# Performance work log

Hardware: AMD Instinct MI355X
Metric: run time of the kernel (lower is better)

The kernel has to match this reference:

```python
import jax, jax.numpy as jnp
import numpy as np

N = 50000
E = 800000
IN = 128
H = 128
C = 64
BN_EPS = 1e-5


def gcn_conv(x, W, b, src, dst, n_nodes):
    # GCNConv: add self-loops, symmetric normalization D^-1/2 (A+I) D^-1/2, linear, bias
    deg = jax.ops.segment_sum(jnp.ones_like(dst, dtype=x.dtype), dst, num_segments=n_nodes)
    dinv = jnp.where(deg > 0, jax.lax.rsqrt(deg), jnp.zeros_like(deg))
    norm = dinv[src] * dinv[dst]                      # [E+N]
    h = x @ W                                         # [N, out]
    agg = jax.ops.segment_sum(norm[:, None] * h[src], dst, num_segments=n_nodes)
    return agg + b


def batch_norm_eval(x, gamma, beta, mean, var):
    return gamma * (x - mean) * jax.lax.rsqrt(var + BN_EPS) + beta


def setup_inputs() -> dict:
    key = jax.random.key(0)
    ks = jax.random.split(key, 16)
    inp = {
        "x": jax.random.normal(ks[0], (N, IN), dtype=jnp.float32),
        "edge_index": jax.random.randint(ks[1], (2, E), 0, N, dtype=jnp.int64),
        "W1": jax.random.normal(ks[2], (IN, H), dtype=jnp.float32) / np.sqrt(IN),
        "b1": jnp.zeros((H,), dtype=jnp.float32),
        "g1": jnp.ones((H,), dtype=jnp.float32),
        "be1": jnp.zeros((H,), dtype=jnp.float32),
        "m1": jax.random.normal(ks[3], (H,), dtype=jnp.float32) * 0.1,
        "v1": jax.random.uniform(ks[4], (H,), dtype=jnp.float32, minval=0.5, maxval=1.5),
        "W2": jax.random.normal(ks[5], (H, H), dtype=jnp.float32) / np.sqrt(H),
        "b2": jnp.zeros((H,), dtype=jnp.float32),
        "g2": jnp.ones((H,), dtype=jnp.float32),
        "be2": jnp.zeros((H,), dtype=jnp.float32),
        "m2": jax.random.normal(ks[6], (H,), dtype=jnp.float32) * 0.1,
        "v2": jax.random.uniform(ks[7], (H,), dtype=jnp.float32, minval=0.5, maxval=1.5),
        "W3": jax.random.normal(ks[8], (H, C), dtype=jnp.float32) / np.sqrt(H),
        "b3": jnp.zeros((C,), dtype=jnp.float32),
    }
    return inp


def reference(x, edge_index, W1, b1, g1, be1, m1, v1, W2, b2, g2, be2, m2, v2, W3, b3):
    # add self loops once (shared across layers, GCNConv cached=True)
    loop = jnp.arange(N, dtype=edge_index.dtype)
    src = jnp.concatenate([edge_index[0], loop])
    dst = jnp.concatenate([edge_index[1], loop])

    h = gcn_conv(x, W1, b1, src, dst, N)
    h = jax.nn.relu(batch_norm_eval(h, g1, be1, m1, v1))  # eval mode: dropout is identity
    h = gcn_conv(h, W2, b2, src, dst, N)
    h = jax.nn.relu(batch_norm_eval(h, g2, be2, m2, v2))
    out = gcn_conv(h, W3, b3, src, dst, N)
    return out
```

## Files before the change

kernel.cpp:

```cpp
#include <hip/hip_runtime.h>


#define NCHUNK 256
#define BSHIFT 8
#define BWID 256
#define NSLAB 8
#define SSHIFT 13
#define ECAP 8192

typedef __attribute__((ext_vector_type(8))) short bf16x8;
typedef __attribute__((ext_vector_type(4))) float f32x4;

__device__ __forceinline__ float blo(unsigned p) { return __uint_as_float(p << 16); }
__device__ __forceinline__ float bhi(unsigned p) { return __uint_as_float(p & 0xffff0000u); }
__device__ __forceinline__ unsigned short f2b(float f) {
  unsigned u = __float_as_uint(f);
  unsigned r = (u + 0x7fffu + ((u >> 16) & 1u)) >> 16;
  return (unsigned short)r;
}

__global__ void wprep_kernel(const float* __restrict__ W1, const float* __restrict__ W2,
                             const float* __restrict__ W3,
                             const float* __restrict__ b1, const float* __restrict__ g1,
                             const float* __restrict__ be1, const float* __restrict__ m1,
                             const float* __restrict__ v1,
                             const float* __restrict__ b2, const float* __restrict__ g2,
                             const float* __restrict__ be2, const float* __restrict__ m2,
                             const float* __restrict__ v2,
                             unsigned short* __restrict__ Wt1,
                             unsigned short* __restrict__ Wt2,
                             unsigned short* __restrict__ Wt3,
                             float* __restrict__ sc1, float* __restrict__ sh1,
                             float* __restrict__ sc2, float* __restrict__ sh2) {
  int i = blockIdx.x * 256 + threadIdx.x;
  if (i < 16384) {
    int k = i >> 7, c = i & 127;
    Wt1[c * 128 + k] = f2b(W1[i]);
  } else if (i < 32768) {
    int j = i - 16384; int k = j >> 7, c = j & 127;
    Wt2[c * 128 + k] = f2b(W2[j]);
  } else if (i < 40960) {
    int j = i - 32768; int k = j >> 6, c = j & 63;
    Wt3[c * 128 + k] = f2b(W3[j]);
  } else if (i < 41088) {
    int c = i - 40960;
    float s = g1[c] * rsqrtf(v1[c] + 1e-5f);
    sc1[c] = s; sh1[c] = (b1[c] - m1[c]) * s + be1[c];
  } else if (i < 41216) {
    int c = i - 41088;
    float s = g2[c] * rsqrtf(v2[c] + 1e-5f);
    sc2[c] = s; sh2[c] = (b2[c] - m2[c]) * s + be2[c];
  }
}

__global__ __launch_bounds__(256) void bin_hist_kernel(
    const int* __restrict__ ei32, const long long* __restrict__ ei64,
    int* __restrict__ counts, int E, int nkeys) {
  __shared__ int hist[2048];
  __shared__ int s_is32;
  int k = blockIdx.x, t = threadIdx.x;
  for (int i = t; i < nkeys; i += 256) hist[i] = 0;
  if (t == 0) s_is32 = 0;
  int CH = (E + NCHUNK - 1) / NCHUNK;
  int e0 = k * CH, e1 = min(e0 + CH, E);
  __syncthreads();
  if (t < 64 && e0 + t < E && ei32[2 * (e0 + t) + 1] != 0) atomicOr(&s_is32, 1);
  __syncthreads();
  int is32 = s_is32;
  for (int e = e0 + t; e < e1; e += 256) {
    int s, d;
    if (is32) { s = ei32[e]; d = ei32[E + e]; }
    else      { s = (int)ei64[e]; d = (int)ei64[E + e]; }
    atomicAdd(&hist[((d >> BSHIFT) << 3) | (s >> SSHIFT)], 1);
  }
  __syncthreads();
  for (int i = t; i < nkeys; i += 256) counts[i * NCHUNK + k] = hist[i];
}

template <int CHUNK>
__global__ __launch_bounds__(256) void scan_partial_kernel(
    const int* __restrict__ src, int* __restrict__ bsum, int n) {
  __shared__ int wsum[4];
  constexpr int EL = CHUNK / 256;
  int b = blockIdx.x, t = threadIdx.x;
  int lane = t & 63, wv = t >> 6;
  int s = 0;
  int i0 = b * CHUNK + t * EL;
#pragma unroll
  for (int q = 0; q < EL / 4; ++q) {
    int i = i0 + q * 4;
    if (i + 3 < n) {
      int4 d4 = *(const int4*)&src[i];
      s += d4.x + d4.y + d4.z + d4.w;
    } else {
      for (int r = 0; r < 4; ++r) if (i + r < n) s += src[i + r];
    }
  }
#pragma unroll
  for (int off = 32; off; off >>= 1) s += __shfl_xor(s, off);
  if (lane == 0) wsum[wv] = s;
  __syncthreads();
  if (t == 0) bsum[b] = wsum[0] + wsum[1] + wsum[2] + wsum[3];
}

template <int CHUNK>
__global__ __launch_bounds__(256) void scan_write_kernel(
    const int* __restrict__ src, const int* __restrict__ bsum,
    int* __restrict__ outp, int n, int nb) {
  constexpr int EL = CHUNK / 256;
  __shared__ int woff[4];
  __shared__ int s_boff;
  int b = blockIdx.x, t = threadIdx.x;
  int lane = t & 63, wv = t >> 6;
  if (t < 64) {
    int v = (t < nb) ? bsum[t] : 0;
    int ic = v;
#pragma unroll
    for (int off = 1; off < 64; off <<= 1) {
      int u = __shfl_up(ic, off);
      if (t >= off) ic += u;
    }
    if (t == b) s_boff = ic - v;
    if (b == nb - 1 && t == 63) outp[n] = ic;
  }
  int vals[EL];
  int i0 = b * CHUNK + t * EL;
#pragma unroll
  for (int q = 0; q < EL / 4; ++q) {
    int i = i0 + q * 4;
    int4 d4 = make_int4(0, 0, 0, 0);
    if (i + 3 < n) d4 = *(const int4*)&src[i];
    else {
      if (i < n) d4.x = src[i];
      if (i + 1 < n) d4.y = src[i + 1];
      if (i + 2 < n) d4.z = src[i + 2];
    }
    vals[q * 4] = d4.x; vals[q * 4 + 1] = d4.y;
    vals[q * 4 + 2] = d4.z; vals[q * 4 + 3] = d4.w;
  }
  int tsum = 0;
#pragma unroll
  for (int q = 0; q < EL; ++q) tsum += vals[q];
  int inc = tsum;
#pragma unroll
  for (int off = 1; off < 64; off <<= 1) {
    int u = __shfl_up(inc, off);
    if (lane >= off) inc += u;
  }
  if (lane == 63) woff[wv] = inc;
  __syncthreads();
  if (t == 0) {
    int r = 0;
#pragma unroll
    for (int w = 0; w < 4; ++w) { int sw = woff[w]; woff[w] = r; r += sw; }
  }
  __syncthreads();
  int p = inc - tsum + woff[wv] + s_boff;
#pragma unroll
  for (int q = 0; q < EL; ++q) {
    int i = i0 + q;
    if (i < n) outp[i] = p;
    p += vals[q];
  }
}

__global__ __launch_bounds__(256) void bin_scatter_kernel(
    const int* __restrict__ ei32, const long long* __restrict__ ei64,
    const int* __restrict__ offs, unsigned* __restrict__ pairs, int E, int nkeys) {
  __shared__ int cur[2048];
  __shared__ int s_is32;
  int k = blockIdx.x, t = threadIdx.x;
  for (int i = t; i < nkeys; i += 256) cur[i] = offs[i * NCHUNK + k];
  if (t == 0) s_is32 = 0;
  int CH = (E + NCHUNK - 1) / NCHUNK;
  int e0 = k * CH, e1 = min(e0 + CH, E);
  __syncthreads();
  if (t < 64 && e0 + t < E && ei32[2 * (e0 + t) + 1] != 0) atomicOr(&s_is32, 1);
  __syncthreads();
  int is32 = s_is32;
  for (int e = e0 + t; e < e1; e += 256) {
    int s, d;
    if (is32) { s = ei32[e]; d = ei32[E + e]; }
    else      { s = (int)ei64[e]; d = (int)ei64[E + e]; }
    int pos = atomicAdd(&cur[((d >> BSHIFT) << 3) | (s >> SSHIFT)], 1);
    pairs[pos] = (unsigned)s | ((unsigned)(d & (BWID - 1)) << 20);
  }
}

__global__ __launch_bounds__(256) void bucket_p1_kernel(
    const unsigned* __restrict__ pairs, const int* __restrict__ offs,
    int* __restrict__ rowptr, float* __restrict__ dinv, int E, int n) {
  __shared__ int deg[BWID];
  __shared__ int woff[4];
  int b = blockIdx.x, t = threadIdx.x;
  int lane = t & 63, wv = t >> 6;
  deg[t] = 0;
  __syncthreads();
  int basep = offs[b * NSLAB * NCHUNK];
  int endp = offs[(b + 1) * NSLAB * NCHUNK];
  for (int i = basep + t; i < endp; i += 256)
    atomicAdd(&deg[pairs[i] >> 20], 1);
  __syncthreads();
  int dg = deg[t];
  int inc = dg + 1;
#pragma unroll
  for (int off = 1; off < 64; off <<= 1) {
    int u = __shfl_up(inc, off);
    if (lane >= off) inc += u;
  }
  if (lane == 63) woff[wv] = inc;
  __syncthreads();
  if (t == 0) {
    int r = 0;
#pragma unroll
    for (int w = 0; w < 4; ++w) { int sw = woff[w]; woff[w] = r; r += sw; }
  }
  __syncthreads();
  int exc = inc - (dg + 1) + woff[wv];
  int cwbase = basep + b * BWID;
  int idx = b * BWID + t;
  if (idx < n) {
    rowptr[idx] = cwbase + exc;
    dinv[idx] = rsqrtf((float)(dg + 1));
  }
  if (b == 0 && t == 0) rowptr[n] = E + n;
}

__global__ __launch_bounds__(256) void bucket_p2_kernel(
    const unsigned* __restrict__ pairs, const int* __restrict__ offs,
    const int* __restrict__ rowptr, const float* __restrict__ dinv,
    uint2* __restrict__ cw, int E, int n) {
  __shared__ int cur[BWID];
  __shared__ float dsl[BWID];
  __shared__ int stage_s[ECAP];
  __shared__ float stage_w[ECAP];
  int b = blockIdx.x, t = threadIdx.x;
  int basep = offs[b * NSLAB * NCHUNK];
  int endp = offs[(b + 1) * NSLAB * NCHUNK];
  int cwbase = basep + b * BWID;
  int idx = b * BWID + t;
  int nreal = min(n - b * BWID, BWID);
  float dv = (t < nreal) ? dinv[idx] : 0.f;
  dsl[t] = dv;
  cur[t] = (t < nreal) ? rowptr[idx] - cwbase : 0;
  __syncthreads();
  if (t < nreal) {
    int pos = atomicAdd(&cur[t], 1);
    if (pos < ECAP) { stage_s[pos] = idx; stage_w[pos] = dv * dv; }
    else cw[cwbase + pos] = make_uint2((unsigned)idx, __float_as_uint(dv * dv));
  }
  __syncthreads();
  for (int i = basep + t; i < endp; i += 256) {
    unsigned p = pairs[i];
    int s = (int)(p & 0xFFFFFu);
    int dl = (int)(p >> 20);
    int pos = atomicAdd(&cur[dl], 1);
    float w = dinv[s] * dsl[dl];
    if (pos < ECAP) { stage_s[pos] = s; stage_w[pos] = w; }
    else cw[cwbase + pos] = make_uint2((unsigned)s, __float_as_uint(w));
  }
  __syncthreads();
  int nE = (endp - basep) + nreal;
  int lim = min(nE, ECAP);
  for (int i = t; i < lim; i += 256)
    cw[cwbase + i] = make_uint2((unsigned)stage_s[i], __float_as_uint(stage_w[i]));
}

template <int HOUT, int ABF16>
__global__ __launch_bounds__(256) void mgemm_kernel(
    const void* __restrict__ Ain, const unsigned short* __restrict__ Wt,
    unsigned short* __restrict__ Y, int n) {
  constexpr int NT = HOUT;
  __shared__ unsigned char AsB[64 * 256];
  __shared__ unsigned char BsB[NT * 256];
  int t = threadIdx.x;
  int row0 = blockIdx.x * 64;

  if constexpr (ABF16) {
    const unsigned short* A = (const unsigned short*)Ain;
#pragma unroll
    for (int jj = 0; jj < 4; ++jj) {
      int f = t + 256 * jj; int r = f >> 4, kq = f & 15;
      uint4 v = make_uint4(0, 0, 0, 0);
      if (row0 + r < n) v = *(const uint4*)&A[(size_t)(row0 + r) * 128 + kq * 8];
      *(uint4*)&AsB[r * 256 + ((kq * 16) ^ ((r & 15) << 4))] = v;
    }
  } else {
    const float* A = (const float*)Ain;
#pragma unroll
    for (int jj = 0; jj < 8; ++jj) {
      int f = t + 256 * jj; int r = f >> 5, kq = f & 31;
      float4 v = make_float4(0.f, 0.f, 0.f, 0.f);
      if (row0 + r < n) v = *(const float4*)&A[(size_t)(row0 + r) * 128 + kq * 4];
      unsigned two0 = (unsigned)f2b(v.x) | ((unsigned)f2b(v.y) << 16);
      unsigned two1 = (unsigned)f2b(v.z) | ((unsigned)f2b(v.w) << 16);
      uint2 o = make_uint2(two0, two1);
      *(uint2*)&AsB[r * 256 + ((kq * 8) ^ ((r & 15) << 4))] = o;
    }
  }
#pragma unroll
  for (int jj = 0; jj < NT / 16; ++jj) {
    int f = t + 256 * jj; int c = f >> 4, kq = f & 15;
    uint4 v = *(const uint4*)&Wt[(size_t)c * 128 + kq * 8];
    *(uint4*)&BsB[c * 256 + ((kq * 16) ^ ((c & 15) << 4))] = v;
  }
  __syncthreads();

  int l = t & 63, wid = t >> 6;
  constexpr int WC = NT / 2;
  constexpr int NI = WC / 16;
  int wr = (wid >> 1) * 32, wc = (wid & 1) * WC;
  int lr = l & 15, lk = (l >> 4) * 16;

  f32x4 acc[2][NI] = {};
#pragma unroll
  for (int ks = 0; ks < 4; ++ks) {
    bf16x8 a[2], b[NI];
#pragma unroll
    for (int mi = 0; mi < 2; ++mi) {
      int r = wr + mi * 16 + lr;
      a[mi] = *(const bf16x8*)&AsB[r * 256 + ((ks * 64 + lk) ^ ((r & 15) << 4))];
    }
#pragma unroll
    for (int ni = 0; ni < NI; ++ni) {
      int c = wc + ni * 16 + lr;
      b[ni] = *(const bf16x8*)&BsB[c * 256 + ((ks * 64 + lk) ^ ((c & 15) << 4))];
    }
#pragma unroll
    for (int mi = 0; mi < 2; ++mi)
#pragma unroll
      for (int ni = 0; ni < NI; ++ni)
        acc[mi][ni] = __builtin_amdgcn_mfma_f32_16x16x32_bf16(a[mi], b[ni],
                                                              acc[mi][ni], 0, 0, 0);
  }

#pragma unroll
  for (int mi = 0; mi < 2; ++mi) {
#pragma unroll
    for (int reg = 0; reg < 4; ++reg) {
      int gr = row0 + wr + mi * 16 + (l >> 4) * 4 + reg;
      if (gr < n) {
#pragma unroll
        for (int ni = 0; ni < NI; ++ni) {
          int gc = wc + ni * 16 + lr;
          Y[(size_t)gr * HOUT + gc] = f2b(acc[mi][ni][reg]);
        }
      }
    }
  }
}

template <int HOUT, bool BN, bool OUTBF>
__global__ __launch_bounds__(256) void agg_kernel(
    const unsigned short* __restrict__ h, const int* __restrict__ rowptr,
    const uint2* __restrict__ cw,
    const float* __restrict__ sc, const float* __restrict__ sh,
    void* __restrict__ out, int n_nodes) {
  int n = (blockIdx.x * blockDim.x + threadIdx.x) >> 6;
  if (n >= n_nodes) return;
  int lane = threadIdx.x & 63;
  constexpr int GL = HOUT / 8;
  constexpr int NPH = 64 / GL;
  int phase = lane / GL;
  int sub = lane & (GL - 1);
  const uint4* hu = (const uint4*)h;

  int beg = rowptr[n], end = rowptr[n + 1];
  float a[8] = {0.f, 0.f, 0.f, 0.f, 0.f, 0.f, 0.f, 0.f};

  int j = beg + phase;
  for (; j + 3 * NPH < end; j += 4 * NPH) {
    uint2 e0 = cw[j], e1 = cw[j + NPH], e2 = cw[j + 2 * NPH], e3 = cw[j + 3 * NPH];
    uint4 h0 = hu[(size_t)e0.x * GL + sub];
    uint4 h1 = hu[(size_t)e1.x * GL + sub];
    uint4 h2 = hu[(size_t)e2.x * GL + sub];
    uint4 h3 = hu[(size_t)e3.x * GL + sub];
    float w0 = __uint_as_float(e0.y), w1 = __uint_as_float(e1.y);
    float w2 = __uint_as_float(e2.y), w3 = __uint_as_float(e3.y);
    a[0] = fmaf(w0, blo(h0.x), a[0]); a[1] = fmaf(w0, bhi(h0.x), a[1]);
    a[2] = fmaf(w0, blo(h0.y), a[2]); a[3] = fmaf(w0, bhi(h0.y), a[3]);
    a[4] = fmaf(w0, blo(h0.z), a[4]); a[5] = fmaf(w0, bhi(h0.z), a[5]);
    a[6] = fmaf(w0, blo(h0.w), a[6]); a[7] = fmaf(w0, bhi(h0.w), a[7]);
    a[0] = fmaf(w1, blo(h1.x), a[0]); a[1] = fmaf(w1, bhi(h1.x), a[1]);
    a[2] = fmaf(w1, blo(h1.y), a[2]); a[3] = fmaf(w1, bhi(h1.y), a[3]);
    a[4] = fmaf(w1, blo(h1.z), a[4]); a[5] = fmaf(w1, bhi(h1.z), a[5]);
    a[6] = fmaf(w1, blo(h1.w), a[6]); a[7] = fmaf(w1, bhi(h1.w), a[7]);
    a[0] = fmaf(w2, blo(h2.x), a[0]); a[1] = fmaf(w2, bhi(h2.x), a[1]);
    a[2] = fmaf(w2, blo(h2.y), a[2]); a[3] = fmaf(w2, bhi(h2.y), a[3]);
    a[4] = fmaf(w2, blo(h2.z), a[4]); a[5] = fmaf(w2, bhi(h2.z), a[5]);
    a[6] = fmaf(w2, blo(h2.w), a[6]); a[7] = fmaf(w2, bhi(h2.w), a[7]);
    a[0] = fmaf(w3, blo(h3.x), a[0]); a[1] = fmaf(w3, bhi(h3.x), a[1]);
    a[2] = fmaf(w3, blo(h3.y), a[2]); a[3] = fmaf(w3, bhi(h3.y), a[3]);
    a[4] = fmaf(w3, blo(h3.z), a[4]); a[5] = fmaf(w3, bhi(h3.z), a[5]);
    a[6] = fmaf(w3, blo(h3.w), a[6]); a[7] = fmaf(w3, bhi(h3.w), a[7]);
  }
  for (; j < end; j += NPH) {
    uint2 e = cw[j];
    uint4 hv = hu[(size_t)e.x * GL + sub];
    float w = __uint_as_float(e.y);
    a[0] = fmaf(w, blo(hv.x), a[0]); a[1] = fmaf(w, bhi(hv.x), a[1]);
    a[2] = fmaf(w, blo(hv.y), a[2]); a[3] = fmaf(w, bhi(hv.y), a[3]);
    a[4] = fmaf(w, blo(hv.z), a[4]); a[5] = fmaf(w, bhi(hv.z), a[5]);
    a[6] = fmaf(w, blo(hv.w), a[6]); a[7] = fmaf(w, bhi(hv.w), a[7]);
  }

#pragma unroll
  for (int q = 0; q < 8; ++q) {
    a[q] += __shfl_xor(a[q], 32);
    a[q] += __shfl_xor(a[q], 16);
    if constexpr (NPH == 8) a[q] += __shfl_xor(a[q], 8);
  }
  if (phase != 0) return;

  int c0 = sub * 8;
  float y[8];
#pragma unroll
  for (int q = 0; q < 8; ++q) {
    if constexpr (BN) y[q] = fmaxf(fmaf(a[q], sc[c0 + q], sh[c0 + q]), 0.f);
    else y[q] = a[q] + sh[c0 + q];
  }
  if constexpr (OUTBF) {
    uint4 o;
    o.x = (unsigned)f2b(y[0]) | ((unsigned)f2b(y[1]) << 16);
    o.y = (unsigned)f2b(y[2]) | ((unsigned)f2b(y[3]) << 16);
    o.z = (unsigned)f2b(y[4]) | ((unsigned)f2b(y[5]) << 16);
    o.w = (unsigned)f2b(y[6]) | ((unsigned)f2b(y[7]) << 16);
    ((uint4*)out)[(size_t)n * GL + sub] = o;
  } else {
    float* op = (float*)out + (size_t)n * HOUT + c0;
    float4 o0; o0.x = y[0]; o0.y = y[1]; o0.z = y[2]; o0.w = y[3];
    float4 o1; o1.x = y[4]; o1.y = y[5]; o1.z = y[6]; o1.w = y[7];
    *(float4*)op = o0;
    *(float4*)(op + 4) = o1;
  }
}

extern "C" void kernel_launch(void* const* d_in, const int* in_sizes, int n_in,
                              void* d_out, int out_size, void* d_ws, size_t ws_size,
                              hipStream_t stream) {
  const float* x = (const float*)d_in[0];
  const int* ei32 = (const int*)d_in[1];
  const long long* ei64 = (const long long*)d_in[1];
  const float* W1 = (const float*)d_in[2];
  const float* b1 = (const float*)d_in[3];
  const float* g1 = (const float*)d_in[4];
  const float* be1 = (const float*)d_in[5];
  const float* m1 = (const float*)d_in[6];
  const float* v1 = (const float*)d_in[7];
  const float* W2 = (const float*)d_in[8];
  const float* b2 = (const float*)d_in[9];
  const float* g2 = (const float*)d_in[10];
  const float* be2 = (const float*)d_in[11];
  const float* m2 = (const float*)d_in[12];
  const float* v2 = (const float*)d_in[13];
  const float* W3 = (const float*)d_in[14];
  const float* b3 = (const float*)d_in[15];

  const int N = in_sizes[0] / 128;
  const int E = in_sizes[1] / 2;
  const int NBK = (N + BWID - 1) / BWID;
  const int NKEYS = NBK * NSLAB;
  const int NC = NKEYS * NCHUNK;

  char* ws = (char*)d_ws;
  size_t off = 0;
  auto alloc = [&](size_t bytes) -> void* {
    void* p = ws + off;
    off = (off + bytes + 255) & ~(size_t)255;
    return p;
  };
  float* dinv = (float*)alloc((size_t)N * 4);
  int* rowptr = (int*)alloc((size_t)(N + 1) * 4);
  int* counts = (int*)alloc((size_t)NC * 4);
  int* offs = (int*)alloc((size_t)(NC + 1) * 4);
  unsigned* pairs = (unsigned*)alloc((size_t)E * 4);
  uint2* cw = (uint2*)alloc((size_t)(E + N) * 8);
  int* bsum = (int*)alloc(64 * 4);
  unsigned short* wt1 = (unsigned short*)alloc(128 * 128 * 2);
  unsigned short* wt2 = (unsigned short*)alloc(128 * 128 * 2);
  unsigned short* wt3 = (unsigned short*)alloc(128 * 64 * 2);
  float* sc1 = (float*)alloc(128 * 4);
  float* sh1 = (float*)alloc(128 * 4);
  float* sc2 = (float*)alloc(128 * 4);
  float* sh2 = (float*)alloc(128 * 4);
  unsigned short* hbuf = (unsigned short*)alloc((size_t)N * 128 * 2);
  unsigned short* ybuf = (unsigned short*)alloc((size_t)N * 128 * 2);
  (void)ws_size;

  wprep_kernel<<<161, 256, 0, stream>>>(W1, W2, W3, b1, g1, be1, m1, v1,
                                        b2, g2, be2, m2, v2,
                                        wt1, wt2, wt3, sc1, sh1, sc2, sh2);

  bin_hist_kernel<<<NCHUNK, 256, 0, stream>>>(ei32, ei64, counts, E, NKEYS);
  int nbC = (NC + 8191) / 8192;
  scan_partial_kernel<8192><<<nbC, 256, 0, stream>>>(counts, bsum, NC);
  scan_write_kernel<8192><<<nbC, 256, 0, stream>>>(counts, bsum, offs, NC, nbC);
  bin_scatter_kernel<<<NCHUNK, 256, 0, stream>>>(ei32, ei64, offs, pairs, E, NKEYS);
  bucket_p1_kernel<<<NBK, 256, 0, stream>>>(pairs, offs, rowptr, dinv, E, N);
  bucket_p2_kernel<<<NBK, 256, 0, stream>>>(pairs, offs, rowptr, dinv, cw, E, N);

  int gb = (N + 63) / 64;
  int ab = (N + 3) / 4;

  mgemm_kernel<128, 0><<<gb, 256, 0, stream>>>(x, wt1, hbuf, N);
  agg_kernel<128, true, true><<<ab, 256, 0, stream>>>(hbuf, rowptr, cw,
                                                      sc1, sh1, ybuf, N);
  mgemm_kernel<128, 1><<<gb, 256, 0, stream>>>(ybuf, wt2, hbuf, N);
  agg_kernel<128, true, true><<<ab, 256, 0, stream>>>(hbuf, rowptr, cw,
                                                      sc2, sh2, ybuf, N);
  mgemm_kernel<64, 1><<<gb, 256, 0, stream>>>(ybuf, wt3, hbuf, N);
  agg_kernel<64, false, false><<<ab, 256, 0, stream>>>(hbuf, rowptr, cw,
                                                       nullptr, b3, d_out, N);
}
```

Baseline: 184.0 us.

## Restructure SpMM aggregation to broadcast edge lists via readlane, lanes span features

The aggregation kernel stops splitting edges across lane groups that each load 16-byte vectors. Instead the wavefront loads up to 64 edge entries cooperatively and broadcasts each one with readlane, so every lane gathers 4 bytes of the neighbour row and keeps only two accumulators. This removes the cross-lane shuffle reduction and the register pressure of eight accumulators per lane. The cost is narrower per-lane loads, more gather instructions per edge, and serial processing of neighbours within a wavefront. The histogram shift is also renamed to a macro without changing its value.

```diff
diff --git a/kernel.cpp b/kernel.cpp
--- a/kernel.cpp
+++ b/kernel.cpp
@@ -6,6 +6,7 @@
 #define BWID 256
 #define NSLAB 8
 #define SSHIFT 13
+#define SLOG 3
 #define ECAP 8192
 
 typedef __attribute__((ext_vector_type(8))) short bf16x8;
@@ -71,7 +72,7 @@
     int s, d;
     if (is32) { s = ei32[e]; d = ei32[E + e]; }
     else      { s = (int)ei64[e]; d = (int)ei64[E + e]; }
-    atomicAdd(&hist[((d >> BSHIFT) << 3) | (s >> SSHIFT)], 1);
+    atomicAdd(&hist[((d >> BSHIFT) << SLOG) | (s >> SSHIFT)], 1);
   }
   __syncthreads();
   for (int i = t; i < nkeys; i += 256) counts[i * NCHUNK + k] = hist[i];
@@ -182,7 +183,7 @@
     int s, d;
     if (is32) { s = ei32[e]; d = ei32[E + e]; }
     else      { s = (int)ei64[e]; d = (int)ei64[E + e]; }
-    int pos = atomicAdd(&cur[((d >> BSHIFT) << 3) | (s >> SSHIFT)], 1);
+    int pos = atomicAdd(&cur[((d >> BSHIFT) << SLOG) | (s >> SSHIFT)], 1);
     pairs[pos] = (unsigned)s | ((unsigned)(d & (BWID - 1)) << 20);
   }
 }
@@ -359,79 +360,103 @@
   int n = (blockIdx.x * blockDim.x + threadIdx.x) >> 6;
   if (n >= n_nodes) return;
   int lane = threadIdx.x & 63;
-  constexpr int GL = HOUT / 8;
-  constexpr int NPH = 64 / GL;
-  int phase = lane / GL;
-  int sub = lane & (GL - 1);
-  const uint4* hu = (const uint4*)h;
-
+  const unsigned* hu = (const unsigned*)h;
   int beg = rowptr[n], end = rowptr[n + 1];
-  float a[8] = {0.f, 0.f, 0.f, 0.f, 0.f, 0.f, 0.f, 0.f};
-
-  int j = beg + phase;
-  for (; j + 3 * NPH < end; j += 4 * NPH) {
-    uint2 e0 = cw[j], e1 = cw[j + NPH], e2 = cw[j + 2 * NPH], e3 = cw[j + 3 * NPH];
-    uint4 h0 = hu[(size_t)e0.x * GL + sub];
-    uint4 h1 = hu[(size_t)e1.x * GL + sub];
-    uint4 h2 = hu[(size_t)e2.x * GL + sub];
-    uint4 h3 = hu[(size_t)e3.x * GL + sub];
-    float w0 = __uint_as_float(e0.y), w1 = __uint_as_float(e1.y);
-    float w2 = __uint_as_float(e2.y), w3 = __uint_as_float(e3.y);
-    a[0] = fmaf(w0, blo(h0.x), a[0]); a[1] = fmaf(w0, bhi(h0.x), a[1]);
-    a[2] = fmaf(w0, blo(h0.y), a[2]); a[3] = fmaf(w0, bhi(h0.y), a[3]);
-    a[4] = fmaf(w0, blo(h0.z), a[4]); a[5] = fmaf(w0, bhi(h0.z), a[5]);
-    a[6] = fmaf(w0, blo(h0.w), a[6]); a[7] = fmaf(w0, bhi(h0.w), a[7]);
-    a[0] = fmaf(w1, blo(h1.x), a[0]); a[1] = fmaf(w1, bhi(h1.x), a[1]);
-    a[2] = fmaf(w1, blo(h1.y), a[2]); a[3] = fmaf(w1, bhi(h1.y), a[3]);
-    a[4] = fmaf(w1, blo(h1.z), a[4]); a[5] = fmaf(w1, bhi(h1.z), a[5]);
-    a[6] = fmaf(w1, blo(h1.w), a[6]); a[7] = fmaf(w1, bhi(h1.w), a[7]);
-    a[0] = fmaf(w2, blo(h2.x), a[0]); a[1] = fmaf(w2, bhi(h2.x), a[1]);
-    a[2] = fmaf(w2, blo(h2.y), a[2]); a[3] = fmaf(w2, bhi(h2.y), a[3]);
-    a[4] = fmaf(w2, blo(h2.z), a[4]); a[5] = fmaf(w2, bhi(h2.z), a[5]);
-    a[6] = fmaf(w2, blo(h2.w), a[6]); a[7] = fmaf(w2, bhi(h2.w), a[7]);
-    a[0] = fmaf(w3, blo(h3.x), a[0]); a[1] = fmaf(w3, bhi(h3.x), a[1]);
-    a[2] = fmaf(w3, blo(h3.y), a[2]); a[3] = fmaf(w3, bhi(h3.y), a[3]);
-    a[4] = fmaf(w3, blo(h3.z), a[4]); a[5] = fmaf(w3, bhi(h3.z), a[5]);
-    a[6] = fmaf(w3, blo(h3.w), a[6]); a[7] = fmaf(w3, bhi(h3.w), a[7]);
-  }
-  for (; j < end; j += NPH) {
-    uint2 e = cw[j];
-    uint4 hv = hu[(size_t)e.x * GL + sub];
-    float w = __uint_as_float(e.y);
-    a[0] = fmaf(w, blo(hv.x), a[0]); a[1] = fmaf(w, bhi(hv.x), a[1]);
-    a[2] = fmaf(w, blo(hv.y), a[2]); a[3] = fmaf(w, bhi(hv.y), a[3]);
-    a[4] = fmaf(w, blo(hv.z), a[4]); a[5] = fmaf(w, bhi(hv.z), a[5]);
-    a[6] = fmaf(w, blo(hv.w), a[6]); a[7] = fmaf(w, bhi(hv.w), a[7]);
-  }
-
-#pragma unroll
-  for (int q = 0; q < 8; ++q) {
-    a[q] += __shfl_xor(a[q], 32);
-    a[q] += __shfl_xor(a[q], 16);
-    if constexpr (NPH == 8) a[q] += __shfl_xor(a[q], 8);
-  }
-  if (phase != 0) return;
-
-  int c0 = sub * 8;
-  float y[8];
-#pragma unroll
-  for (int q = 0; q < 8; ++q) {
-    if constexpr (BN) y[q] = fmaxf(fmaf(a[q], sc[c0 + q], sh[c0 + q]), 0.f);
-    else y[q] = a[q] + sh[c0 + q];
-  }
-  if constexpr (OUTBF) {
-    uint4 o;
-    o.x = (unsigned)f2b(y[0]) | ((unsigned)f2b(y[1]) << 16);
-    o.y = (unsigned)f2b(y[2]) | ((unsigned)f2b(y[3]) << 16);
-    o.z = (unsigned)f2b(y[4]) | ((unsigned)f2b(y[5]) << 16);
-    o.w = (unsigned)f2b(y[6]) | ((unsigned)f2b(y[7]) << 16);
-    ((uint4*)out)[(size_t)n * GL + sub] = o;
+  int deg = end - beg;
+
+  float acc0 = 0.f, acc1 = 0.f;
+
+  if constexpr (HOUT == 128) {
+    for (int j0 = 0; j0 < deg; j0 += 64) {
+      int ii = beg + j0 + lane;
+      ii = ii < end ? ii : end - 1;
+      uint2 sv = cw[ii];
+      int cnt = min(64, deg - j0);
+      int j = 0;
+      for (; j + 3 < cnt; j += 4) {
+        unsigned s0 = __builtin_amdgcn_readlane(sv.x, j);
+        unsigned u0 = __builtin_amdgcn_readlane(sv.y, j);
+        unsigned s1 = __builtin_amdgcn_readlane(sv.x, j + 1);
+        unsigned u1 = __builtin_amdgcn_readlane(sv.y, j + 1);
+        unsigned s2 = __builtin_amdgcn_readlane(sv.x, j + 2);
+        unsigned u2 = __builtin_amdgcn_readlane(sv.y, j + 2);
+        unsigned s3 = __builtin_amdgcn_readlane(sv.x, j + 3);
+        unsigned u3 = __builtin_amdgcn_readlane(sv.y, j + 3);
+        unsigned v0 = hu[(size_t)s0 * 64 + lane];
+        unsigned v1 = hu[(size_t)s1 * 64 + lane];
+        unsigned v2 = hu[(size_t)s2 * 64 + lane];
+        unsigned v3 = hu[(size_t)s3 * 64 + lane];
+        float w0 = __uint_as_float(u0), w1 = __uint_as_float(u1);
+        float w2 = __uint_as_float(u2), w3 = __uint_as_float(u3);
+        acc0 = fmaf(w0, blo(v0), acc0); acc1 = fmaf(w0, bhi(v0), acc1);
+        acc0 = fmaf(w1, blo(v1), acc0); acc1 = fmaf(w1, bhi(v1), acc1);
+        acc0 = fmaf(w2, blo(v2), acc0); acc1 = fmaf(w2, bhi(v2), acc1);
+        acc0 = fmaf(w3, blo(v3), acc0); acc1 = fmaf(w3, bhi(v3), acc1);
+      }
+      for (; j < cnt; ++j) {
+        unsigned s = __builtin_amdgcn_readlane(sv.x, j);
+        unsigned u = __builtin_amdgcn_readlane(sv.y, j);
+        unsigned v = hu[(size_t)s * 64 + lane];
+        float w = __uint_as_float(u);
+        acc0 = fmaf(w, blo(v), acc0);
+        acc1 = fmaf(w, bhi(v), acc1);
+      }
+    }
+    int c0 = lane * 2;
+    float y0, y1;
+    if constexpr (BN) {
+      y0 = fmaxf(fmaf(acc0, sc[c0], sh[c0]), 0.f);
+      y1 = fmaxf(fmaf(acc1, sc[c0 + 1], sh[c0 + 1]), 0.f);
+    } else {
+      y0 = acc0 + sh[c0];
+      y1 = acc1 + sh[c0 + 1];
+    }
+    if constexpr (OUTBF) {
+      unsigned pk = (unsigned)f2b(y0) | ((unsigned)f2b(y1) << 16);
+      ((unsigned*)out)[(size_t)n * 64 + lane] = pk;
+    } else {
+      float2 o; o.x = y0; o.y = y1;
+      *(float2*)&((float*)out)[(size_t)n * 128 + c0] = o;
+    }
   } else {
-    float* op = (float*)out + (size_t)n * HOUT + c0;
-    float4 o0; o0.x = y[0]; o0.y = y[1]; o0.z = y[2]; o0.w = y[3];
-    float4 o1; o1.x = y[4]; o1.y = y[5]; o1.z = y[6]; o1.w = y[7];
-    *(float4*)op = o0;
-    *(float4*)(op + 4) = o1;
+    int half = lane >> 5, hl = lane & 31;
+    for (int j0 = 0; j0 < deg; j0 += 64) {
+      int ii = beg + j0 + lane;
+      ii = ii < end ? ii : end - 1;
+      uint2 sv = cw[ii];
+      int cnt = min(64, deg - j0);
+      for (int j = 0; j < cnt; j += 2) {
+        unsigned sA = __builtin_amdgcn_readlane(sv.x, j);
+        unsigned uA = __builtin_amdgcn_readlane(sv.y, j);
+        int j1 = (j + 1 < cnt) ? j + 1 : j;
+        unsigned sB = __builtin_amdgcn_readlane(sv.x, j1);
+        unsigned uB = (j + 1 < cnt) ? __builtin_amdgcn_readlane(sv.y, j1) : 0u;
+        unsigned s = half ? sB : sA;
+        float w = __uint_as_float(half ? uB : uA);
+        unsigned v = hu[(size_t)s * 32 + hl];
+        acc0 = fmaf(w, blo(v), acc0);
+        acc1 = fmaf(w, bhi(v), acc1);
+      }
+    }
+    acc0 += __shfl_xor(acc0, 32);
+    acc1 += __shfl_xor(acc1, 32);
+    if (half != 0) return;
+    int c0 = hl * 2;
+    float y0, y1;
+    if constexpr (BN) {
+      y0 = fmaxf(fmaf(acc0, sc[c0], sh[c0]), 0.f);
+      y1 = fmaxf(fmaf(acc1, sc[c0 + 1], sh[c0 + 1]), 0.f);
+    } else {
+      y0 = acc0 + sh[c0];
+      y1 = acc1 + sh[c0 + 1];
+    }
+    if constexpr (OUTBF) {
+      unsigned pk = (unsigned)f2b(y0) | ((unsigned)f2b(y1) << 16);
+      ((unsigned*)out)[(size_t)n * 32 + hl] = pk;
+    } else {
+      float2 o; o.x = y0; o.y = y1;
+      *(float2*)&((float*)out)[(size_t)n * 64 + c0] = o;
+    }
   }
 }
 
```

Result: slower. 195.1 us (+6.0%).

## Split aggregation by column groups and drop source-slab binning of edges

Applied to the files above, without the earlier changes.

The aggregation kernel now divides the feature columns into 8 column groups, with 8 consecutive blocks handling the same nodes in different column groups. Each lane gathers one 32-bit word (two bf16 values) per edge instead of a 16-byte vector. The likely intent is to localise the gathered slice of h per column group in cache and to spread work more evenly across blocks. Edge binning is simplified to bin by destination bucket only, removing the source-slab sub-keys, which shrinks the histogram and scan sizes. The trade-off is that each edge list is re-read once per column group, the gathers become narrow, and source locality within a destination bucket is lost.

```diff
diff --git a/kernel.cpp b/kernel.cpp
--- a/kernel.cpp
+++ b/kernel.cpp
@@ -4,8 +4,6 @@
 #define NCHUNK 256
 #define BSHIFT 8
 #define BWID 256
-#define NSLAB 8
-#define SSHIFT 13
 #define ECAP 8192
 
 typedef __attribute__((ext_vector_type(8))) short bf16x8;
@@ -55,11 +53,11 @@
 
 __global__ __launch_bounds__(256) void bin_hist_kernel(
     const int* __restrict__ ei32, const long long* __restrict__ ei64,
-    int* __restrict__ counts, int E, int nkeys) {
-  __shared__ int hist[2048];
+    int* __restrict__ counts, int E, int nbk) {
+  __shared__ int hist[BWID];
   __shared__ int s_is32;
   int k = blockIdx.x, t = threadIdx.x;
-  for (int i = t; i < nkeys; i += 256) hist[i] = 0;
+  hist[t] = 0;
   if (t == 0) s_is32 = 0;
   int CH = (E + NCHUNK - 1) / NCHUNK;
   int e0 = k * CH, e1 = min(e0 + CH, E);
@@ -68,13 +66,11 @@
   __syncthreads();
   int is32 = s_is32;
   for (int e = e0 + t; e < e1; e += 256) {
-    int s, d;
-    if (is32) { s = ei32[e]; d = ei32[E + e]; }
-    else      { s = (int)ei64[e]; d = (int)ei64[E + e]; }
-    atomicAdd(&hist[((d >> BSHIFT) << 3) | (s >> SSHIFT)], 1);
-  }
-  __syncthreads();
-  for (int i = t; i < nkeys; i += 256) counts[i * NCHUNK + k] = hist[i];
+    int d = is32 ? ei32[E + e] : (int)ei64[E + e];
+    atomicAdd(&hist[d >> BSHIFT], 1);
+  }
+  __syncthreads();
+  if (t < nbk) counts[t * NCHUNK + k] = hist[t];
 }
 
 template <int CHUNK>
@@ -166,11 +162,11 @@
 
 __global__ __launch_bounds__(256) void bin_scatter_kernel(
     const int* __restrict__ ei32, const long long* __restrict__ ei64,
-    const int* __restrict__ offs, unsigned* __restrict__ pairs, int E, int nkeys) {
-  __shared__ int cur[2048];
+    const int* __restrict__ offs, unsigned* __restrict__ pairs, int E, int nbk) {
+  __shared__ int cur[BWID];
   __shared__ int s_is32;
   int k = blockIdx.x, t = threadIdx.x;
-  for (int i = t; i < nkeys; i += 256) cur[i] = offs[i * NCHUNK + k];
+  if (t < nbk) cur[t] = offs[t * NCHUNK + k];
   if (t == 0) s_is32 = 0;
   int CH = (E + NCHUNK - 1) / NCHUNK;
   int e0 = k * CH, e1 = min(e0 + CH, E);
@@ -182,7 +178,7 @@
     int s, d;
     if (is32) { s = ei32[e]; d = ei32[E + e]; }
     else      { s = (int)ei64[e]; d = (int)ei64[E + e]; }
-    int pos = atomicAdd(&cur[((d >> BSHIFT) << 3) | (s >> SSHIFT)], 1);
+    int pos = atomicAdd(&cur[d >> BSHIFT], 1);
     pairs[pos] = (unsigned)s | ((unsigned)(d & (BWID - 1)) << 20);
   }
 }
@@ -196,8 +192,8 @@
   int lane = t & 63, wv = t >> 6;
   deg[t] = 0;
   __syncthreads();
-  int basep = offs[b * NSLAB * NCHUNK];
-  int endp = offs[(b + 1) * NSLAB * NCHUNK];
+  int basep = offs[b * NCHUNK];
+  int endp = offs[(b + 1) * NCHUNK];
   for (int i = basep + t; i < endp; i += 256)
     atomicAdd(&deg[pairs[i] >> 20], 1);
   __syncthreads();
@@ -235,8 +231,8 @@
   __shared__ int stage_s[ECAP];
   __shared__ float stage_w[ECAP];
   int b = blockIdx.x, t = threadIdx.x;
-  int basep = offs[b * NSLAB * NCHUNK];
-  int endp = offs[(b + 1) * NSLAB * NCHUNK];
+  int basep = offs[b * NCHUNK];
+  int endp = offs[(b + 1) * NCHUNK];
   int cwbase = basep + b * BWID;
   int idx = b * BWID + t;
   int nreal = min(n - b * BWID, BWID);
@@ -356,82 +352,70 @@
     const uint2* __restrict__ cw,
     const float* __restrict__ sc, const float* __restrict__ sh,
     void* __restrict__ out, int n_nodes) {
-  int n = (blockIdx.x * blockDim.x + threadIdx.x) >> 6;
-  if (n >= n_nodes) return;
+  constexpr int RWU = HOUT / 2;
+  int grp = blockIdx.x & 7;
+  int blk = blockIdx.x >> 3;
+  int wv = threadIdx.x >> 6;
   int lane = threadIdx.x & 63;
-  constexpr int GL = HOUT / 8;
-  constexpr int NPH = 64 / GL;
-  int phase = lane / GL;
-  int sub = lane & (GL - 1);
-  const uint4* hu = (const uint4*)h;
-
-  int beg = rowptr[n], end = rowptr[n + 1];
-  float a[8] = {0.f, 0.f, 0.f, 0.f, 0.f, 0.f, 0.f, 0.f};
-
-  int j = beg + phase;
-  for (; j + 3 * NPH < end; j += 4 * NPH) {
-    uint2 e0 = cw[j], e1 = cw[j + NPH], e2 = cw[j + 2 * NPH], e3 = cw[j + 3 * NPH];
-    uint4 h0 = hu[(size_t)e0.x * GL + sub];
-    uint4 h1 = hu[(size_t)e1.x * GL + sub];
-    uint4 h2 = hu[(size_t)e2.x * GL + sub];
-    uint4 h3 = hu[(size_t)e3.x * GL + sub];
-    float w0 = __uint_as_float(e0.y), w1 = __uint_as_float(e1.y);
-    float w2 = __uint_as_float(e2.y), w3 = __uint_as_float(e3.y);
-    a[0] = fmaf(w0, blo(h0.x), a[0]); a[1] = fmaf(w0, bhi(h0.x), a[1]);
-    a[2] = fmaf(w0, blo(h0.y), a[2]); a[3] = fmaf(w0, bhi(h0.y), a[3]);
-    a[4] = fmaf(w0, blo(h0.z), a[4]); a[5] = fmaf(w0, bhi(h0.z), a[5]);
-    a[6] = fmaf(w0, blo(h0.w), a[6]); a[7] = fmaf(w0, bhi(h0.w), a[7]);
-    a[0] = fmaf(w1, blo(h1.x), a[0]); a[1] = fmaf(w1, bhi(h1.x), a[1]);
-    a[2] = fmaf(w1, blo(h1.y), a[2]); a[3] = fmaf(w1, bhi(h1.y), a[3]);
-    a[4] = fmaf(w1, blo(h1.z), a[4]); a[5] = fmaf(w1, bhi(h1.z), a[5]);
-    a[6] = fmaf(w1, blo(h1.w), a[6]); a[7] = fmaf(w1, bhi(h1.w), a[7]);
-    a[0] = fmaf(w2, blo(h2.x), a[0]); a[1] = fmaf(w2, bhi(h2.x), a[1]);
-    a[2] = fmaf(w2, blo(h2.y), a[2]); a[3] = fmaf(w2, bhi(h2.y), a[3]);
-    a[4] = fmaf(w2, blo(h2.z), a[4]); a[5] = fmaf(w2, bhi(h2.z), a[5]);
-    a[6] = fmaf(w2, blo(h2.w), a[6]); a[7] = fmaf(w2, bhi(h2.w), a[7]);
-    a[0] = fmaf(w3, blo(h3.x), a[0]); a[1] = fmaf(w3, bhi(h3.x), a[1]);
-    a[2] = fmaf(w3, blo(h3.y), a[2]); a[3] = fmaf(w3, bhi(h3.y), a[3]);
-    a[4] = fmaf(w3, blo(h3.z), a[4]); a[5] = fmaf(w3, bhi(h3.z), a[5]);
-    a[6] = fmaf(w3, blo(h3.w), a[6]); a[7] = fmaf(w3, bhi(h3.w), a[7]);
-  }
-  for (; j < end; j += NPH) {
-    uint2 e = cw[j];
-    uint4 hv = hu[(size_t)e.x * GL + sub];
-    float w = __uint_as_float(e.y);
-    a[0] = fmaf(w, blo(hv.x), a[0]); a[1] = fmaf(w, bhi(hv.x), a[1]);
-    a[2] = fmaf(w, blo(hv.y), a[2]); a[3] = fmaf(w, bhi(hv.y), a[3]);
-    a[4] = fmaf(w, blo(hv.z), a[4]); a[5] = fmaf(w, bhi(hv.z), a[5]);
-    a[6] = fmaf(w, blo(hv.w), a[6]); a[7] = fmaf(w, bhi(hv.w), a[7]);
-  }
-
-#pragma unroll
-  for (int q = 0; q < 8; ++q) {
-    a[q] += __shfl_xor(a[q], 32);
-    a[q] += __shfl_xor(a[q], 16);
-    if constexpr (NPH == 8) a[q] += __shfl_xor(a[q], 8);
-  }
-  if (phase != 0) return;
-
-  int c0 = sub * 8;
-  float y[8];
-#pragma unroll
-  for (int q = 0; q < 8; ++q) {
-    if constexpr (BN) y[q] = fmaxf(fmaf(a[q], sc[c0 + q], sh[c0 + q]), 0.f);
-    else y[q] = a[q] + sh[c0 + q];
-  }
-  if constexpr (OUTBF) {
-    uint4 o;
-    o.x = (unsigned)f2b(y[0]) | ((unsigned)f2b(y[1]) << 16);
-    o.y = (unsigned)f2b(y[2]) | ((unsigned)f2b(y[3]) << 16);
-    o.z = (unsigned)f2b(y[4]) | ((unsigned)f2b(y[5]) << 16);
-    o.w = (unsigned)f2b(y[6]) | ((unsigned)f2b(y[7]) << 16);
-    ((uint4*)out)[(size_t)n * GL + sub] = o;
+  int phase = lane >> 3;
+  int sub = lane & 7;
+  int cg, n0;
+  if constexpr (HOUT == 128) {
+    cg = grp;
+    n0 = blk * 8 + wv * 2;
   } else {
-    float* op = (float*)out + (size_t)n * HOUT + c0;
-    float4 o0; o0.x = y[0]; o0.y = y[1]; o0.z = y[2]; o0.w = y[3];
-    float4 o1; o1.x = y[4]; o1.y = y[5]; o1.z = y[6]; o1.w = y[7];
-    *(float4*)op = o0;
-    *(float4*)(op + 4) = o1;
+    cg = grp >> 1;
+    n0 = (blk * 2 + (grp & 1)) * 8 + wv * 2;
+  }
+  const unsigned* hu = (const unsigned*)h;
+  int cbase = cg * 8;
+
+#pragma unroll
+  for (int ni = 0; ni < 2; ++ni) {
+    int n = n0 + ni;
+    if (n >= n_nodes) continue;
+    int beg = rowptr[n], end = rowptr[n + 1];
+    float a0 = 0.f, a1 = 0.f;
+    for (int j = beg; j < end; j += 32) {
+      int j0 = j + phase, j1 = j0 + 8, j2 = j0 + 16, j3 = j0 + 24;
+      uint2 e0 = cw[j0 < end ? j0 : end - 1];
+      uint2 e1 = cw[j1 < end ? j1 : end - 1];
+      uint2 e2 = cw[j2 < end ? j2 : end - 1];
+      uint2 e3 = cw[j3 < end ? j3 : end - 1];
+      unsigned v0 = hu[(size_t)e0.x * RWU + cbase + sub];
+      unsigned v1 = hu[(size_t)e1.x * RWU + cbase + sub];
+      unsigned v2 = hu[(size_t)e2.x * RWU + cbase + sub];
+      unsigned v3 = hu[(size_t)e3.x * RWU + cbase + sub];
+      float w0 = (j0 < end) ? __uint_as_float(e0.y) : 0.f;
+      float w1 = (j1 < end) ? __uint_as_float(e1.y) : 0.f;
+      float w2 = (j2 < end) ? __uint_as_float(e2.y) : 0.f;
+      float w3 = (j3 < end) ? __uint_as_float(e3.y) : 0.f;
+      a0 = fmaf(w0, blo(v0), a0); a1 = fmaf(w0, bhi(v0), a1);
+      a0 = fmaf(w1, blo(v1), a0); a1 = fmaf(w1, bhi(v1), a1);
+      a0 = fmaf(w2, blo(v2), a0); a1 = fmaf(w2, bhi(v2), a1);
+      a0 = fmaf(w3, blo(v3), a0); a1 = fmaf(w3, bhi(v3), a1);
+    }
+    a0 += __shfl_xor(a0, 32); a1 += __shfl_xor(a1, 32);
+    a0 += __shfl_xor(a0, 16); a1 += __shfl_xor(a1, 16);
+    a0 += __shfl_xor(a0, 8);  a1 += __shfl_xor(a1, 8);
+    if (phase == 0) {
+      int c0 = (cbase + sub) * 2;
+      float y0, y1;
+      if constexpr (BN) {
+        y0 = fmaxf(fmaf(a0, sc[c0], sh[c0]), 0.f);
+        y1 = fmaxf(fmaf(a1, sc[c0 + 1], sh[c0 + 1]), 0.f);
+      } else {
+        y0 = a0 + sh[c0];
+        y1 = a1 + sh[c0 + 1];
+      }
+      if constexpr (OUTBF) {
+        unsigned pk = (unsigned)f2b(y0) | ((unsigned)f2b(y1) << 16);
+        ((unsigned*)out)[(size_t)n * RWU + cbase + sub] = pk;
+      } else {
+        float2 o; o.x = y0; o.y = y1;
+        *(float2*)&((float*)out)[(size_t)n * HOUT + c0] = o;
+      }
+    }
   }
 }
 
@@ -459,8 +443,7 @@
   const int N = in_sizes[0] / 128;
   const int E = in_sizes[1] / 2;
   const int NBK = (N + BWID - 1) / BWID;
-  const int NKEYS = NBK * NSLAB;
-  const int NC = NKEYS * NCHUNK;
+  const int NC = NBK * NCHUNK;
 
   char* ws = (char*)d_ws;
   size_t off = 0;
@@ -491,24 +474,26 @@
                                         b2, g2, be2, m2, v2,
                                         wt1, wt2, wt3, sc1, sh1, sc2, sh2);
 
-  bin_hist_kernel<<<NCHUNK, 256, 0, stream>>>(ei32, ei64, counts, E, NKEYS);
+  bin_hist_kernel<<<NCHUNK, 256, 0, stream>>>(ei32, ei64, counts, E, NBK);
   int nbC = (NC + 8191) / 8192;
   scan_partial_kernel<8192><<<nbC, 256, 0, stream>>>(counts, bsum, NC);
   scan_write_kernel<8192><<<nbC, 256, 0, stream>>>(counts, bsum, offs, NC, nbC);
-  bin_scatter_kernel<<<NCHUNK, 256, 0, stream>>>(ei32, ei64, offs, pairs, E, NKEYS);
+  bin_scatter_kernel<<<NCHUNK, 256, 0, stream>>>(ei32, ei64, offs, pairs, E, NBK);
   bucket_p1_kernel<<<NBK, 256, 0, stream>>>(pairs, offs, rowptr, dinv, E, N);
   bucket_p2_kernel<<<NBK, 256, 0, stream>>>(pairs, offs, rowptr, dinv, cw, E, N);
 
   int gb = (N + 63) / 64;
-  int ab = (N + 3) / 4;
+  int chunks = (N + 7) / 8;
+  int ag128 = chunks * 8;
+  int ag64 = ((chunks + 1) / 2) * 8;
 
   mgemm_kernel<128, 0><<<gb, 256, 0, stream>>>(x, wt1, hbuf, N);
-  agg_kernel<128, true, true><<<ab, 256, 0, stream>>>(hbuf, rowptr, cw,
-                                                      sc1, sh1, ybuf, N);
+  agg_kernel<128, true, true><<<ag128, 256, 0, stream>>>(hbuf, rowptr, cw,
+                                                         sc1, sh1, ybuf, N);
   mgemm_kernel<128, 1><<<gb, 256, 0, stream>>>(ybuf, wt2, hbuf, N);
-  agg_kernel<128, true, true><<<ab, 256, 0, stream>>>(hbuf, rowptr, cw,
-                                                      sc2, sh2, ybuf, N);
+  agg_kernel<128, true, true><<<ag128, 256, 0, stream>>>(hbuf, rowptr, cw,
+                                                         sc2, sh2, ybuf, N);
   mgemm_kernel<64, 1><<<gb, 256, 0, stream>>>(ybuf, wt3, hbuf, N);
-  agg_kernel<64, false, false><<<ab, 256, 0, stream>>>(hbuf, rowptr, cw,
-                                                       nullptr, b3, d_out, N);
-}
+  agg_kernel<64, false, false><<<ag64, 256, 0, stream>>>(hbuf, rowptr, cw,
+                                                         nullptr, b3, d_out, N);
+}
```

New measurement: 343.9 us. +86.8%, slower.
